# Performance work log

Hardware: AMD Instinct MI355X
Metric: run time of the kernel (lower is better)

## Reference

```python
import jax, jax.numpy as jnp
import numpy as np

BS, NQ, D = 4, 12500, 256
HEADS, LEVELS, POINTS = 8, 2, 4
HD = D // HEADS
D_FF = 2048
SHAPES = ((100, 100), (50, 50))   # (H, W) per level; sum(H*W) == NQ
STARTS = (0, 10000)


def layer_norm(x, g, b, eps=1e-5):
    m = x.mean(-1, keepdims=True)
    v = ((x - m) ** 2).mean(-1, keepdims=True)
    return (x - m) * jax.lax.rsqrt(v + eps) * g + b


def bilinear_sample(value_l, loc, H, W):
    # value_l: (bs, heads, H*W, hd); loc: (bs, heads, nq, P, 2) normalized [0,1]
    # matches F.grid_sample(align_corners=False, padding_mode='zeros')
    x = loc[..., 0] * W - 0.5
    y = loc[..., 1] * H - 0.5
    x0 = jnp.floor(x)
    y0 = jnp.floor(y)
    wx1 = x - x0
    wy1 = y - y0
    wx0 = 1.0 - wx1
    wy0 = 1.0 - wy1
    x0i = x0.astype(jnp.int32)
    y0i = y0.astype(jnp.int32)

    def gather(xi, yi):
        valid = (xi >= 0) & (xi < W) & (yi >= 0) & (yi < H)
        idx = jnp.clip(yi, 0, H - 1) * W + jnp.clip(xi, 0, W - 1)  # (bs,heads,nq,P)
        b, h, nq, P = idx.shape
        g = jnp.take_along_axis(value_l, idx.reshape(b, h, nq * P, 1), axis=2)
        g = g.reshape(b, h, nq, P, -1)
        return g * valid[..., None].astype(g.dtype)

    g00 = gather(x0i, y0i)
    g10 = gather(x0i + 1, y0i)
    g01 = gather(x0i, y0i + 1)
    g11 = gather(x0i + 1, y0i + 1)
    return (g00 * (wx0 * wy0)[..., None] + g10 * (wx1 * wy0)[..., None]
            + g01 * (wx0 * wy1)[..., None] + g11 * (wx1 * wy1)[..., None])


def setup_inputs() -> dict:
    key = jax.random.key(0)
    ks = jax.random.split(key, 20)
    s = 0.02
    inp = {
        'query': jax.random.normal(ks[0], (BS, NQ, D), jnp.float32),
        'reference_points': jax.random.uniform(ks[1], (BS, NQ, LEVELS, 2), jnp.float32),
        'w_off': s * jax.random.normal(ks[2], (D, HEADS * LEVELS * POINTS * 2), jnp.float32),
        'b_off': s * jax.random.normal(ks[3], (HEADS * LEVELS * POINTS * 2,), jnp.float32),
        'w_attn': s * jax.random.normal(ks[4], (D, HEADS * LEVELS * POINTS), jnp.float32),
        'b_attn': s * jax.random.normal(ks[5], (HEADS * LEVELS * POINTS,), jnp.float32),
        'w_val': s * jax.random.normal(ks[6], (D, D), jnp.float32),
        'b_val': jnp.zeros((D,), jnp.float32),
        'w_out': s * jax.random.normal(ks[7], (D, D), jnp.float32),
        'b_out': jnp.zeros((D,), jnp.float32),
        'w1': s * jax.random.normal(ks[8], (D, D_FF), jnp.float32),
        'b1': jnp.zeros((D_FF,), jnp.float32),
        'w2': s * jax.random.normal(ks[9], (D_FF, D), jnp.float32),
        'b2': jnp.zeros((D,), jnp.float32),
        'ln0_g': jnp.ones((D,), jnp.float32),
        'ln0_b': jnp.zeros((D,), jnp.float32),
        'ln1_g': jnp.ones((D,), jnp.float32),
        'ln1_b': jnp.zeros((D,), jnp.float32),
    }
    return inp


def reference(query, reference_points, w_off, b_off, w_attn, b_attn, w_val, b_val,
              w_out, b_out, w1, b1, w2, b2, ln0_g, ln0_b, ln1_g, ln1_b):
    bs, nq, _ = query.shape
    # value projection; encoder self-attention: value == query tokens
    value = (query @ w_val + b_val).reshape(bs, nq, HEADS, HD).transpose(0, 2, 1, 3)  # (bs,heads,nv,hd)
    off = (query @ w_off + b_off).reshape(bs, nq, HEADS, LEVELS, POINTS, 2)
    aw = (query @ w_attn + b_attn).reshape(bs, nq, HEADS, LEVELS * POINTS)
    aw = jax.nn.softmax(aw, axis=-1).reshape(bs, nq, HEADS, LEVELS, POINTS)

    out = jnp.zeros((bs, HEADS, nq, HD), query.dtype)
    for l, (H, W) in enumerate(SHAPES):
        normalizer = jnp.array([W, H], query.dtype)
        # (bs,nq,heads,P,2)
        loc = reference_points[:, :, None, l, None, :] + off[:, :, :, l] / normalizer
        loc = loc.transpose(0, 2, 1, 3, 4)  # (bs,heads,nq,P,2)
        v_l = value[:, :, STARTS[l]:STARTS[l] + H * W]  # (bs,heads,H*W,hd)
        sampled = bilinear_sample(v_l, loc, H, W)       # (bs,heads,nq,P,hd)
        w_l = aw[:, :, :, l].transpose(0, 2, 1, 3)      # (bs,heads,nq,P)
        out = out + (sampled * w_l[..., None]).sum(axis=3)

    attn_out = out.transpose(0, 2, 1, 3).reshape(bs, nq, D) @ w_out + b_out
    x = layer_norm(query + attn_out, ln0_g, ln0_b)
    h = jax.nn.relu(x @ w1 + b1)
    x = layer_norm(x + (h @ w2 + b2), ln1_g, ln1_b)
    return x
```

## Files before the change

### kernel.cpp

```cpp
#include <hip/hip_runtime.h>


#define NQv 12500
#define BSv 4
#define Dv  256
#define DFF 2048

typedef __attribute__((ext_vector_type(8))) __bf16 bf16x8;
typedef __attribute__((ext_vector_type(4))) float f32x4;

__device__ __forceinline__ ushort f32_to_bf16(float f) {
  unsigned u = __float_as_uint(f);
  u += 0x7FFFu + ((u >> 16) & 1u);
  return (ushort)(u >> 16);
}
__device__ __forceinline__ float bf16_to_f32(ushort u) {
  return __uint_as_float(((unsigned)u) << 16);
}

__global__ __launch_bounds__(256) void conv_bf16_kernel(
    const float* __restrict__ in, ushort* __restrict__ out, int n4) {
  int i = blockIdx.x * 256 + threadIdx.x;
  if (i >= n4) return;
  float4 v = reinterpret_cast<const float4*>(in)[i];
  uint2 st;
  st.x = (unsigned)f32_to_bf16(v.x) | ((unsigned)f32_to_bf16(v.y) << 16);
  st.y = (unsigned)f32_to_bf16(v.z) | ((unsigned)f32_to_bf16(v.w) << 16);
  reinterpret_cast<uint2*>(out)[i] = st;
}

__global__ __launch_bounds__(256) void ttrans_kernel(
    const float* __restrict__ in, ushort* __restrict__ out, int K, int N) {
  __shared__ ushort tl[64][65];
  const int n0 = blockIdx.x * 64, k0 = blockIdx.y * 64;
  const int t = threadIdx.x;
#pragma unroll
  for (int i = 0; i < 16; ++i) {
    int idx = t + 256 * i;
    int r = idx >> 6, c = idx & 63;
    tl[r][c] = f32_to_bf16(in[(size_t)(k0 + r) * N + n0 + c]);
  }
  __syncthreads();
#pragma unroll
  for (int i = 0; i < 16; ++i) {
    int idx = t + 256 * i;
    int r = idx >> 6, c = idx & 63;
    out[(size_t)(n0 + r) * K + k0 + c] = tl[c][r];
  }
}

__global__ __launch_bounds__(256) void build_wcat_kernel(
    const float* __restrict__ w_val, const float* __restrict__ w_off,
    const float* __restrict__ w_attn, const float* __restrict__ b_val,
    const float* __restrict__ b_off, const float* __restrict__ b_attn,
    ushort* __restrict__ wcat, float* __restrict__ bcat) {
  int i = blockIdx.x * 256 + threadIdx.x;
  if (i < 448 * 256) {
    int n = i >> 8, k = i & 255;
    float v = (n < 256) ? w_val[(size_t)k * 256 + n]
              : (n < 384) ? w_off[(size_t)k * 128 + (n - 256)]
                          : w_attn[(size_t)k * 64 + (n - 384)];
    wcat[i] = f32_to_bf16(v);
  }
  if (i < 512)
    bcat[i] = (i < 256) ? b_val[i] : (i < 384) ? b_off[i - 256]
              : (i < 448) ? b_attn[i - 384] : 0.f;
}

#define TBM 128
#define TBN 128
#define TBK 32

template <int RELU, int NMASK>
__global__ __launch_bounds__(256) void gemm128_kernel(
    const ushort* __restrict__ A, const ushort* __restrict__ Bt,
    const float* __restrict__ bias, ushort* __restrict__ C,
    int M, int K, int ldc, int Nreal) {
  __shared__ ushort lds[4][TBM * TBK];

  const int t = threadIdx.x;
  const int wid = t >> 6, lane = t & 63;
  const int wr = wid >> 1, wc = wid & 1;
  const int m0 = blockIdx.y * TBM;
  const int n0 = blockIdx.x * TBN;

  int srowA[2], srowB[2], gsl[2];
#pragma unroll
  for (int i = 0; i < 2; i++) {
    int row = i * 64 + (t >> 2);
    int ar = m0 + row;
    srowA[i] = (ar < M) ? ar : (M - 1);
    srowB[i] = n0 + row;
    gsl[i] = ((t & 3) ^ ((row >> 1) & 3)) * 8;
  }

  f32x4 acc[4][4] = {};
  const int nt = K / TBK;
  int cur = 0;

#pragma unroll
  for (int i = 0; i < 2; i++) {
    const int ldsoff = (i * 256 + wid * 64) * 8;
    __builtin_amdgcn_global_load_lds(
        (const __attribute__((address_space(1))) void*)(A + (size_t)srowA[i] * K + gsl[i]),
        (__attribute__((address_space(3))) void*)(lds[0] + ldsoff), 16, 0, 0);
    __builtin_amdgcn_global_load_lds(
        (const __attribute__((address_space(1))) void*)(Bt + (size_t)srowB[i] * K + gsl[i]),
        (__attribute__((address_space(3))) void*)(lds[1] + ldsoff), 16, 0, 0);
  }
  __syncthreads();

  const int rl = lane & 15, kh = lane >> 4;
  for (int tk = 0; tk < nt; ++tk) {
    if (tk + 1 < nt) {
      const int k0 = (tk + 1) * TBK;
      const int nb = (cur ^ 1) * 2;
#pragma unroll
      for (int i = 0; i < 2; i++) {
        const int ldsoff = (i * 256 + wid * 64) * 8;
        __builtin_amdgcn_global_load_lds(
            (const __attribute__((address_space(1))) void*)(A + (size_t)srowA[i] * K + k0 + gsl[i]),
            (__attribute__((address_space(3))) void*)(lds[nb] + ldsoff), 16, 0, 0);
        __builtin_amdgcn_global_load_lds(
            (const __attribute__((address_space(1))) void*)(Bt + (size_t)srowB[i] * K + k0 + gsl[i]),
            (__attribute__((address_space(3))) void*)(lds[nb + 1] + ldsoff), 16, 0, 0);
      }
    }
    {
      const ushort* As = lds[cur * 2];
      const ushort* Bs = lds[cur * 2 + 1];
      bf16x8 afr[4], bfr[4];
#pragma unroll
      for (int ni = 0; ni < 4; ni++) {
        int rowb = wc * 64 + ni * 16 + rl;
        int p = kh ^ ((rowb >> 1) & 3);
        bfr[ni] = *reinterpret_cast<const bf16x8*>(Bs + rowb * 32 + p * 8);
      }
#pragma unroll
      for (int mi = 0; mi < 4; mi++) {
        int rowa = wr * 64 + mi * 16 + rl;
        int p = kh ^ ((rowa >> 1) & 3);
        afr[mi] = *reinterpret_cast<const bf16x8*>(As + rowa * 32 + p * 8);
      }
#pragma unroll
      for (int mi = 0; mi < 4; mi++)
#pragma unroll
        for (int ni = 0; ni < 4; ni++)
          acc[mi][ni] = __builtin_amdgcn_mfma_f32_16x16x32_bf16(afr[mi], bfr[ni], acc[mi][ni], 0, 0, 0);
    }
    __syncthreads();
    cur ^= 1;
  }

  ushort* ldsC = lds[0];
  const int rgrp = lane >> 4, cl = lane & 15;
#pragma unroll
  for (int pass = 0; pass < 2; ++pass) {
    if (wr == pass) {
#pragma unroll
      for (int mi = 0; mi < 4; mi++) {
#pragma unroll
        for (int ni = 0; ni < 4; ni++) {
          int col = wc * 64 + ni * 16 + cl;
          float bv = bias[n0 + col];
#pragma unroll
          for (int r = 0; r < 4; r++) {
            int rloc = mi * 16 + rgrp * 4 + r;
            float v = acc[mi][ni][r] + bv;
            if (RELU) v = fmaxf(v, 0.f);
            ldsC[rloc * 132 + col] = f32_to_bf16(v);
          }
        }
      }
    }
    __syncthreads();
    {
      int rloc = t >> 2;
      int row = m0 + pass * 64 + rloc;
      if (row < M) {
#pragma unroll
        for (int j = 0; j < 4; j++) {
          int col = (t & 3) * 32 + j * 8;
          if (!NMASK || n0 + col < Nreal) {
            uint4 v = *reinterpret_cast<const uint4*>(ldsC + rloc * 132 + col);
            *reinterpret_cast<uint4*>(C + (size_t)row * ldc + n0 + col) = v;
          }
        }
      }
    }
    __syncthreads();
  }
}

__global__ __launch_bounds__(256, 2) void outproj_ln0_kernel(
    const ushort* __restrict__ samp,
    const ushort* __restrict__ wqt,
    const float* __restrict__ bias,
    const float* __restrict__ query,
    const float* __restrict__ g0, const float* __restrict__ be0,
    ushort* __restrict__ xb,
    int M) {
  __shared__ ushort lds_all[32768];
  ushort* As = lds_all;
  ushort* ring0 = lds_all + 16384;

  const int t = threadIdx.x;
  const int wv = t >> 6;
  const int lane = t & 63;
  const int rl = lane & 15, kq = lane >> 4;
  const int cl = lane & 15, g4 = lane >> 4;
  const int m0 = blockIdx.x * 64;

  ushort* ring[2] = {ring0, ring0 + 8192};

  auto issueB = [&](int j, ushort* dst) {
#pragma unroll
    for (int ii = 0; ii < 4; ++ii) {
      int row = (t >> 2) + 64 * ii;
      int g = (t & 3) ^ ((row >> 1) & 3);
      __builtin_amdgcn_global_load_lds(
          (const __attribute__((address_space(1))) void*)(
              wqt + (size_t)row * 256 + j * 32 + g * 8),
          (__attribute__((address_space(3))) void*)(dst + ((size_t)t + 256 * ii) * 8), 16, 0, 0);
    }
  };

#pragma unroll
  for (int ii = 0; ii < 8; ++ii) {
    int row = (t >> 5) + 8 * ii;
    int g = (t & 31) ^ (row & 7);
    int ar = m0 + row; ar = (ar < M) ? ar : (M - 1);
    __builtin_amdgcn_global_load_lds(
        (const __attribute__((address_space(1))) void*)(samp + (size_t)ar * 256 + g * 8),
        (__attribute__((address_space(3))) void*)(As + ((size_t)t + 256 * ii) * 8), 16, 0, 0);
  }
  issueB(0, ring[0]);
  __syncthreads();

  f32x4 accF[4][4] = {};
  int cur = 0;

#pragma unroll
  for (int j = 0; j < 8; ++j) {
    if (j + 1 < 8) issueB(j + 1, ring[cur ^ 1]);
    const ushort* Bs = ring[cur];
    bf16x8 afr[4], bfr[4];
    const int slotA = j * 4 + kq;
#pragma unroll
    for (int mi = 0; mi < 4; mi++) {
      int rowa = mi * 16 + rl;
      afr[mi] = *reinterpret_cast<const bf16x8*>(As + rowa * 256 + (slotA ^ (rowa & 7)) * 8);
    }
#pragma unroll
    for (int ni = 0; ni < 4; ni++) {
      int rowb = wv * 64 + ni * 16 + rl;
      bfr[ni] = *reinterpret_cast<const bf16x8*>(Bs + rowb * 32 + (kq ^ ((rowb >> 1) & 3)) * 8);
    }
    __builtin_amdgcn_s_setprio(1);
#pragma unroll
    for (int mi = 0; mi < 4; mi++)
#pragma unroll
      for (int ni = 0; ni < 4; ni++)
        accF[mi][ni] = __builtin_amdgcn_mfma_f32_16x16x32_bf16(afr[mi], bfr[ni], accF[mi][ni], 0, 0, 0);
    __builtin_amdgcn_s_setprio(0);
    __syncthreads();
    cur ^= 1;
  }

  float* ptab = (float*)ring0;
  float* mtab = (float*)(ring0 + 2048);

  float bc[4], gc[4], bec[4];
#pragma unroll
  for (int ni = 0; ni < 4; ni++) {
    int col = wv * 64 + ni * 16 + cl;
    bc[ni] = bias[col]; gc[ni] = g0[col]; bec[ni] = be0[col];
  }
#pragma unroll
  for (int mi = 0; mi < 4; mi++) {
#pragma unroll
    for (int ni = 0; ni < 4; ni++) {
      int col = wv * 64 + ni * 16 + cl;
#pragma unroll
      for (int r = 0; r < 4; r++) {
        int row = mi * 16 + g4 * 4 + r;
        int qrow = m0 + row; qrow = (qrow < M) ? qrow : (M - 1);
        accF[mi][ni][r] += bc[ni] + query[(size_t)qrow * 256 + col];
      }
    }
  }
#pragma unroll
  for (int mi = 0; mi < 4; mi++) {
#pragma unroll
    for (int r = 0; r < 4; r++) {
      float s = accF[mi][0][r] + accF[mi][1][r] + accF[mi][2][r] + accF[mi][3][r];
      float sq = accF[mi][0][r] * accF[mi][0][r] + accF[mi][1][r] * accF[mi][1][r] +
                 accF[mi][2][r] * accF[mi][2][r] + accF[mi][3][r] * accF[mi][3][r];
#pragma unroll
      for (int o = 1; o < 16; o <<= 1) {
        s += __shfl_xor(s, o, 64);
        sq += __shfl_xor(sq, o, 64);
      }
      if (cl == 0) {
        int row = mi * 16 + g4 * 4 + r;
        ptab[(row * 4 + wv) * 2 + 0] = s;
        ptab[(row * 4 + wv) * 2 + 1] = sq;
      }
    }
  }
  __syncthreads();
  {
    int row = t >> 2, part = t & 3;
    float s = ptab[(row * 4 + part) * 2 + 0];
    float sq = ptab[(row * 4 + part) * 2 + 1];
    s += __shfl_xor(s, 1, 64);  sq += __shfl_xor(sq, 1, 64);
    s += __shfl_xor(s, 2, 64);  sq += __shfl_xor(sq, 2, 64);
    if (part == 0) {
      float mean = s * (1.f / 256.f);
      float var = sq * (1.f / 256.f) - mean * mean;
      mtab[row * 2 + 0] = mean;
      mtab[row * 2 + 1] = rsqrtf(var + 1e-5f);
    }
  }
  __syncthreads();
#pragma unroll
  for (int mi = 0; mi < 4; mi++) {
#pragma unroll
    for (int r = 0; r < 4; r++) {
      int row = mi * 16 + g4 * 4 + r;
      float2 ms = *reinterpret_cast<const float2*>(mtab + row * 2);
      int grow = m0 + row;
      if (grow < M) {
#pragma unroll
        for (int ni = 0; ni < 4; ni++) {
          int col = wv * 64 + ni * 16 + cl;
          xb[(size_t)grow * 256 + col] =
              f32_to_bf16((accF[mi][ni][r] - ms.x) * ms.y * gc[ni] + bec[ni]);
        }
      }
    }
  }
}

__global__ __launch_bounds__(512, 1) void ffn_ln_fused_kernel(
    const ushort* __restrict__ xb,
    const ushort* __restrict__ w1t,
    const float* __restrict__ b1,
    const ushort* __restrict__ w2t,
    const float* __restrict__ b2,
    const float* __restrict__ g1, const float* __restrict__ be1,
    float* __restrict__ out,
    int M) {
  __shared__ ushort lds_all[74752];
  ushort* As = lds_all;
  ushort* Hs = lds_all + 32768;
  ushort* stg0 = lds_all + 50176;

  const int t = threadIdx.x;
  const int wv = t >> 6;
  const int wm = wv >> 2;
  const int wn = wv & 3;
  const int lane = t & 63;
  const int rl = lane & 15, kq = lane >> 4;
  const int cl = lane & 15, g4 = lane >> 4;
  const int m0 = blockIdx.x * 128;

  const int b1row = t >> 3, b1slot = t & 7;
  const int b2row = t >> 2, b2slot = t & 3;

  auto stg = [&](int i) { return stg0 + i * 8192; };

  auto issueB1 = [&](int p, int j, ushort* dst) {
#pragma unroll
    for (int ii = 0; ii < 2; ++ii) {
      int row = b1row + 64 * ii;
      int g = b1slot ^ (row & 7);
      __builtin_amdgcn_global_load_lds(
          (const __attribute__((address_space(1))) void*)(
              w1t + (size_t)(p * 128 + row) * 256 + j * 64 + g * 8),
          (__attribute__((address_space(3))) void*)(dst + (t + 512 * ii) * 8), 16, 0, 0);
    }
  };
  auto issueB2 = [&](int p, int tt, ushort* dst) {
#pragma unroll
    for (int ii = 0; ii < 2; ++ii) {
      int row = b2row + 128 * ii;
      int g = b2slot ^ ((row >> 1) & 3);
      __builtin_amdgcn_global_load_lds(
          (const __attribute__((address_space(1))) void*)(
              w2t + (size_t)row * 2048 + p * 128 + tt * 32 + g * 8),
          (__attribute__((address_space(3))) void*)(dst + (t + 512 * ii) * 8), 16, 0, 0);
    }
  };

#pragma unroll
  for (int ii = 0; ii < 8; ++ii) {
    int row = (t >> 5) + 16 * ii;
    int g = (t & 31) ^ (row & 7);
    int ar = m0 + row; ar = (ar < M) ? ar : (M - 1);
    __builtin_amdgcn_global_load_lds(
        (const __attribute__((address_space(1))) void*)(xb + (size_t)ar * 256 + g * 8),
        (__attribute__((address_space(3))) void*)(As + (t + 512 * ii) * 8), 16, 0, 0);
  }
  issueB1(0, 0, stg(0));
  issueB1(0, 1, stg(1));
  asm volatile("s_waitcnt vmcnt(2)" ::: "memory");
  __builtin_amdgcn_s_barrier();

  f32x4 acc1[4][2] = {};
  f32x4 accF[4][4] = {};
  int cur = 0;

  for (int p = 0; p < 16; ++p) {
#pragma unroll
    for (int j = 0; j < 8; ++j) {
      int tgt = cur + 2; if (tgt >= 3) tgt -= 3;
      if (j <= 5) {
        const int j2 = j + 2;
        const int p2 = p + (j2 >> 3);
        if ((j2 & 7) < 4) issueB1(p2, j2 & 3, stg(tgt));
        else issueB2(p2, (j2 & 7) - 4, stg(tgt));
        asm volatile("s_waitcnt vmcnt(4) lgkmcnt(0)" ::: "memory");
      } else if (p < 15) {
        const int j2m = (j + 2) & 7;
        issueB1(p + 1, j2m, stg(tgt));
        asm volatile("s_waitcnt vmcnt(4) lgkmcnt(0)" ::: "memory");
      } else if (j == 6) {
        asm volatile("s_waitcnt vmcnt(2) lgkmcnt(0)" ::: "memory");
      } else {
        asm volatile("s_waitcnt vmcnt(0) lgkmcnt(0)" ::: "memory");
      }
      __builtin_amdgcn_s_barrier();
      __builtin_amdgcn_sched_barrier(0);

      const ushort* Bs = stg(cur);
      if (j < 4) {
        __builtin_amdgcn_s_setprio(1);
#pragma unroll
        for (int kk = 0; kk < 2; ++kk) {
          bf16x8 afr[4], bfr[2];
          const int slotA = j * 8 + kk * 4 + kq;
#pragma unroll
          for (int mi = 0; mi < 4; mi++) {
            int rowa = wm * 64 + mi * 16 + rl;
            afr[mi] = *reinterpret_cast<const bf16x8*>(As + rowa * 256 + (slotA ^ (rowa & 7)) * 8);
          }
          const int slotB = kk * 4 + kq;
#pragma unroll
          for (int ni = 0; ni < 2; ni++) {
            int rowb = wn * 32 + ni * 16 + rl;
            bfr[ni] = *reinterpret_cast<const bf16x8*>(Bs + rowb * 64 + (slotB ^ (rowb & 7)) * 8);
          }
#pragma unroll
          for (int mi = 0; mi < 4; mi++)
#pragma unroll
            for (int ni = 0; ni < 2; ni++)
              acc1[mi][ni] = __builtin_amdgcn_mfma_f32_16x16x32_bf16(afr[mi], bfr[ni], acc1[mi][ni], 0, 0, 0);
        }
        __builtin_amdgcn_s_setprio(0);
        if (j == 3) {
#pragma unroll
          for (int ni = 0; ni < 2; ni++) {
            int col = wn * 32 + ni * 16 + cl;
            float b1v = b1[p * 128 + col];
#pragma unroll
            for (int mi = 0; mi < 4; mi++) {
#pragma unroll
              for (int r = 0; r < 4; r++) {
                int row = wm * 64 + mi * 16 + g4 * 4 + r;
                Hs[row * 136 + col] = f32_to_bf16(fmaxf(acc1[mi][ni][r] + b1v, 0.f));
              }
            }
          }
#pragma unroll
          for (int mi = 0; mi < 4; mi++)
#pragma unroll
            for (int ni = 0; ni < 2; ni++)
              acc1[mi][ni] = (f32x4){0.f, 0.f, 0.f, 0.f};
        }
      } else {
        const int tt = j - 4;
        bf16x8 a2f[4], b2f[4];
#pragma unroll
        for (int mi = 0; mi < 4; mi++) {
          int rowa = wm * 64 + mi * 16 + rl;
          a2f[mi] = *reinterpret_cast<const bf16x8*>(Hs + rowa * 136 + (tt * 4 + kq) * 8);
        }
#pragma unroll
        for (int ni = 0; ni < 4; ni++) {
          int rowb = wn * 64 + ni * 16 + rl;
          b2f[ni] = *reinterpret_cast<const bf16x8*>(Bs + rowb * 32 + (kq ^ ((rowb >> 1) & 3)) * 8);
        }
        __builtin_amdgcn_s_setprio(1);
#pragma unroll
        for (int mi = 0; mi < 4; mi++)
#pragma unroll
          for (int ni = 0; ni < 4; ni++)
            accF[mi][ni] = __builtin_amdgcn_mfma_f32_16x16x32_bf16(a2f[mi], b2f[ni], accF[mi][ni], 0, 0, 0);
        __builtin_amdgcn_s_setprio(0);
      }
      cur = cur + 1; if (cur >= 3) cur -= 3;
    }
  }

  float* ptab = (float*)stg0;
  float* mtab = (float*)(stg0 + 2048);

  float b2c[4], g1c[4], bec[4];
#pragma unroll
  for (int ni = 0; ni < 4; ni++) {
    int col = wn * 64 + ni * 16 + cl;
    b2c[ni] = b2[col]; g1c[ni] = g1[col]; bec[ni] = be1[col];
  }
#pragma unroll
  for (int mi = 0; mi < 4; mi++) {
#pragma unroll
    for (int ni = 0; ni < 4; ni++) {
      int col = wn * 64 + ni * 16 + cl;
#pragma unroll
      for (int r = 0; r < 4; r++) {
        int row = wm * 64 + mi * 16 + g4 * 4 + r;
        ushort xv = As[row * 256 + ((col >> 3) ^ (row & 7)) * 8 + (col & 7)];
        accF[mi][ni][r] += b2c[ni] + bf16_to_f32(xv);
      }
    }
  }
#pragma unroll
  for (int mi = 0; mi < 4; mi++) {
#pragma unroll
    for (int r = 0; r < 4; r++) {
      float s = accF[mi][0][r] + accF[mi][1][r] + accF[mi][2][r] + accF[mi][3][r];
      float sq = accF[mi][0][r] * accF[mi][0][r] + accF[mi][1][r] * accF[mi][1][r] +
                 accF[mi][2][r] * accF[mi][2][r] + accF[mi][3][r] * accF[mi][3][r];
#pragma unroll
      for (int o = 1; o < 16; o <<= 1) {
        s += __shfl_xor(s, o, 64);
        sq += __shfl_xor(sq, o, 64);
      }
      if (cl == 0) {
        int row = wm * 64 + mi * 16 + g4 * 4 + r;
        ptab[(row * 4 + wn) * 2 + 0] = s;
        ptab[(row * 4 + wn) * 2 + 1] = sq;
      }
    }
  }
  __syncthreads();
  {
    int row = t >> 2, part = t & 3;
    float s = ptab[(row * 4 + part) * 2 + 0];
    float sq = ptab[(row * 4 + part) * 2 + 1];
    s += __shfl_xor(s, 1, 64);  sq += __shfl_xor(sq, 1, 64);
    s += __shfl_xor(s, 2, 64);  sq += __shfl_xor(sq, 2, 64);
    if (part == 0) {
      float mean = s * (1.f / 256.f);
      float var = sq * (1.f / 256.f) - mean * mean;
      mtab[row * 2 + 0] = mean;
      mtab[row * 2 + 1] = rsqrtf(var + 1e-5f);
    }
  }
  __syncthreads();
#pragma unroll
  for (int mi = 0; mi < 4; mi++) {
#pragma unroll
    for (int r = 0; r < 4; r++) {
      int row = wm * 64 + mi * 16 + g4 * 4 + r;
      float2 ms = *reinterpret_cast<const float2*>(mtab + row * 2);
      int grow = m0 + row;
      if (grow < M) {
#pragma unroll
        for (int ni = 0; ni < 4; ni++) {
          int col = wn * 64 + ni * 16 + cl;
          out[(size_t)grow * 256 + col] = (accF[mi][ni][r] - ms.x) * ms.y * g1c[ni] + bec[ni];
        }
      }
    }
  }
}

__global__ __launch_bounds__(256) void deform_attn_kernel(
    const ushort* __restrict__ pcat, const float* __restrict__ refp,
    ushort* __restrict__ out, int total) {
  int tid = blockIdx.x * 256 + threadIdx.x;
  if (tid >= total) return;
  int c0 = (tid & 3) * 8;
  int idx = tid >> 2;
  int h = idx & 7;
  int row = idx >> 3;
  int bl = row / NQv;

  const ushort* prow = pcat + (size_t)row * 448;

  ushort awr[8];
  *reinterpret_cast<uint4*>(awr) = *reinterpret_cast<const uint4*>(prow + 384 + h * 8);
  float lg[8], mx = -1e30f;
#pragma unroll
  for (int i = 0; i < 8; i++) { lg[i] = bf16_to_f32(awr[i]); mx = fmaxf(mx, lg[i]); }
  float ssum = 0.f;
#pragma unroll
  for (int i = 0; i < 8; i++) { lg[i] = __expf(lg[i] - mx); ssum += lg[i]; }
  float inv = 1.f / ssum;

  ushort ofr[16];
  *reinterpret_cast<uint4*>(ofr)     = *reinterpret_cast<const uint4*>(prow + 256 + h * 16);
  *reinterpret_cast<uint4*>(ofr + 8) = *reinterpret_cast<const uint4*>(prow + 256 + h * 16 + 8);
  float4 rp = *reinterpret_cast<const float4*>(refp + (size_t)row * 4);

  float acc8[8] = {};
  const int Ws[2] = {100, 50}, Hs2[2] = {100, 50}, Ss[2] = {0, 10000};
#pragma unroll
  for (int l = 0; l < 2; l++) {
    const int W = Ws[l], H = Hs2[l];
    float fx = (l ? rp.z : rp.x) * (float)W - 0.5f;
    float fy = (l ? rp.w : rp.y) * (float)H - 0.5f;
    const ushort* vbase = pcat + ((size_t)bl * NQv + Ss[l]) * 448 + h * 32 + c0;
#pragma unroll
    for (int p = 0; p < 4; p++) {
      float x = fx + bf16_to_f32(ofr[l * 8 + p * 2 + 0]);
      float y = fy + bf16_to_f32(ofr[l * 8 + p * 2 + 1]);
      float x0f = floorf(x), y0f = floorf(y);
      float wx1 = x - x0f, wy1 = y - y0f;
      float wx0 = 1.f - wx1, wy0 = 1.f - wy1;
      int x0 = (int)x0f, y0 = (int)y0f;
      float aw = lg[l * 4 + p] * inv;

      float cw[4] = {aw * wx0 * wy0, aw * wx1 * wy0, aw * wx0 * wy1, aw * wx1 * wy1};
      int cx[4] = {x0, x0 + 1, x0, x0 + 1};
      int cy[4] = {y0, y0, y0 + 1, y0 + 1};
#pragma unroll
      for (int c = 0; c < 4; c++) {
        int xi = cx[c], yi = cy[c];
        if (xi >= 0 && xi < W && yi >= 0 && yi < H) {
          ushort vr[8];
          *reinterpret_cast<uint4*>(vr) =
              *reinterpret_cast<const uint4*>(vbase + (size_t)(yi * W + xi) * 448);
          float w = cw[c];
#pragma unroll
          for (int j = 0; j < 8; j++) acc8[j] += w * bf16_to_f32(vr[j]);
        }
      }
    }
  }

  ushort st[8];
#pragma unroll
  for (int j = 0; j < 8; j++) st[j] = f32_to_bf16(acc8[j]);
  *reinterpret_cast<uint4*>(out + (size_t)row * 256 + h * 32 + c0) =
      *reinterpret_cast<uint4*>(st);
}

extern "C" void kernel_launch(void* const* d_in, const int* in_sizes, int n_in,
                              void* d_out, int out_size, void* d_ws, size_t ws_size,
                              hipStream_t stream) {
  const float* query  = (const float*)d_in[0];
  const float* refp   = (const float*)d_in[1];
  const float* w_off  = (const float*)d_in[2];
  const float* b_off  = (const float*)d_in[3];
  const float* w_attn = (const float*)d_in[4];
  const float* b_attn = (const float*)d_in[5];
  const float* w_val  = (const float*)d_in[6];
  const float* b_val  = (const float*)d_in[7];
  const float* w_out  = (const float*)d_in[8];
  const float* b_out  = (const float*)d_in[9];
  const float* w1     = (const float*)d_in[10];
  const float* b1     = (const float*)d_in[11];
  const float* w2     = (const float*)d_in[12];
  const float* b2     = (const float*)d_in[13];
  const float* ln0g   = (const float*)d_in[14];
  const float* ln0b   = (const float*)d_in[15];
  const float* ln1g   = (const float*)d_in[16];
  const float* ln1b   = (const float*)d_in[17];
  float* outp = (float*)d_out;

  char* ws = (char*)d_ws;
  size_t woff = 0;
  auto walloc = [&](size_t bytes) { size_t r = woff; woff += (bytes + 255) & ~(size_t)255; return r; };
  ushort* wcat = (ushort*)(ws + walloc((size_t)512 * 256 * 2));
  float*  bcat = (float*)(ws + walloc(512 * 4));
  ushort* wqt  = (ushort*)(ws + walloc((size_t)256 * 256 * 2));
  ushort* w1t  = (ushort*)(ws + walloc((size_t)DFF * 256 * 2));
  ushort* w2t  = (ushort*)(ws + walloc((size_t)256 * DFF * 2));
  char* arena = ws + woff;
  size_t arena_sz = (ws_size > woff) ? (ws_size - woff) : 0;

  int nb = ((size_t)BSv * NQv * 1920 + (1u << 20) <= arena_sz) ? BSv : 1;
  const int R = nb * NQv;
  ushort* qb   = (ushort*)arena;
  ushort* pcat = (ushort*)(arena + (size_t)R * 512);
  ushort* samp = (ushort*)(arena + (size_t)R * 1408);
  ushort* xb   = qb;

  build_wcat_kernel<<<dim3(448), dim3(256), 0, stream>>>(
      w_val, w_off, w_attn, b_val, b_off, b_attn, wcat, bcat);
  ttrans_kernel<<<dim3(4, 4), dim3(256), 0, stream>>>(w_out, wqt, Dv, Dv);
  ttrans_kernel<<<dim3(DFF / 64, 4), dim3(256), 0, stream>>>(w1, w1t, Dv, DFF);
  ttrans_kernel<<<dim3(4, DFF / 64), dim3(256), 0, stream>>>(w2, w2t, DFF, Dv);

  const int MT = (R + TBM - 1) / TBM;

  for (int c = 0; c < BSv / nb; c++) {
    const int row0 = c * R;
    const float* qrow = query + (size_t)row0 * Dv;

    conv_bf16_kernel<<<dim3((R * 64 + 255) / 256), dim3(256), 0, stream>>>(qrow, qb, R * 64);

    gemm128_kernel<0, 1><<<dim3(4, MT), dim3(256), 0, stream>>>(
        qb, wcat, bcat, pcat, R, Dv, 448, 448);

    deform_attn_kernel<<<dim3((R * 32 + 255) / 256), dim3(256), 0, stream>>>(
        pcat, refp + (size_t)row0 * 4, samp, R * 32);

    outproj_ln0_kernel<<<dim3((R + 63) / 64), dim3(256), 0, stream>>>(
        samp, wqt, b_out, qrow, ln0g, ln0b, xb, R);

    ffn_ln_fused_kernel<<<dim3((R + 127) / 128), dim3(512), 0, stream>>>(
        xb, w1t, b1, w2t, b2, ln1g, ln1b, outp + (size_t)row0 * 256, R);
  }
}
```

Baseline: 328.9 us.

## Split value and offset/attn projections into separate buffers; share sampling work via shuffles

The fused projection GEMM now writes the value projection into a dense 256-wide buffer and the offsets plus attention logits into a separate 192-wide buffer, in place of one 448-wide interleaved array. Value gathers in the deformable attention kernel therefore stride 256 elements instead of 448, which packs sampled rows more tightly for cache and TLB. Each of the four lanes serving a head now loads only its share of offsets and logits, and the softmax and sample coordinates are exchanged with wave shuffles. This removes redundant per-lane loads and softmax work at the cost of extra shuffle instructions.

```diff
diff --git a/kernel.cpp b/kernel.cpp
--- a/kernel.cpp
+++ b/kernel.cpp
@@ -71,10 +71,11 @@
 #define TBN 128
 #define TBK 32
 
-template <int RELU, int NMASK>
+template <int RELU, int NMASK, int SPLIT>
 __global__ __launch_bounds__(256) void gemm128_kernel(
     const ushort* __restrict__ A, const ushort* __restrict__ Bt,
     const float* __restrict__ bias, ushort* __restrict__ C,
+    ushort* __restrict__ C2,
     int M, int K, int ldc, int Nreal) {
   __shared__ ushort lds[4][TBM * TBK];
 
@@ -181,8 +182,14 @@
 #pragma unroll
         for (int j = 0; j < 4; j++) {
           int col = (t & 3) * 32 + j * 8;
-          if (!NMASK || n0 + col < Nreal) {
-            uint4 v = *reinterpret_cast<const uint4*>(ldsC + rloc * 132 + col);
+          uint4 v = *reinterpret_cast<const uint4*>(ldsC + rloc * 132 + col);
+          if (SPLIT) {
+            int gcol = n0 + col;
+            if (gcol < 256)
+              *reinterpret_cast<uint4*>(C + (size_t)row * 256 + gcol) = v;
+            else if (gcol < 448)
+              *reinterpret_cast<uint4*>(C2 + (size_t)row * 192 + (gcol - 256)) = v;
+          } else if (!NMASK || n0 + col < Nreal) {
             *reinterpret_cast<uint4*>(C + (size_t)row * ldc + n0 + col) = v;
           }
         }
@@ -343,14 +350,10 @@
 }
 
 __global__ __launch_bounds__(512, 1) void ffn_ln_fused_kernel(
-    const ushort* __restrict__ xb,
-    const ushort* __restrict__ w1t,
-    const float* __restrict__ b1,
-    const ushort* __restrict__ w2t,
-    const float* __restrict__ b2,
-    const float* __restrict__ g1, const float* __restrict__ be1,
-    float* __restrict__ out,
-    int M) {
+    const ushort* __restrict__ xb, const ushort* __restrict__ w1t,
+    const float* __restrict__ b1, const ushort* __restrict__ w2t,
+    const float* __restrict__ b2, const float* __restrict__ g1,
+    const float* __restrict__ be1, float* __restrict__ out, int M) {
   __shared__ ushort lds_all[74752];
   ushort* As = lds_all;
   ushort* Hs = lds_all + 32768;
@@ -578,65 +581,73 @@
 }
 
 __global__ __launch_bounds__(256) void deform_attn_kernel(
-    const ushort* __restrict__ pcat, const float* __restrict__ refp,
-    ushort* __restrict__ out, int total) {
+    const ushort* __restrict__ val,
+    const ushort* __restrict__ oa,
+    const float* __restrict__ refp,
+    ushort* __restrict__ out,
+    int total)
+{
   int tid = blockIdx.x * 256 + threadIdx.x;
   if (tid >= total) return;
-  int c0 = (tid & 3) * 8;
+  int c = tid & 3;
   int idx = tid >> 2;
   int h = idx & 7;
   int row = idx >> 3;
   int bl = row / NQv;
 
-  const ushort* prow = pcat + (size_t)row * 448;
-
-  ushort awr[8];
-  *reinterpret_cast<uint4*>(awr) = *reinterpret_cast<const uint4*>(prow + 384 + h * 8);
-  float lg[8], mx = -1e30f;
-#pragma unroll
-  for (int i = 0; i < 8; i++) { lg[i] = bf16_to_f32(awr[i]); mx = fmaxf(mx, lg[i]); }
-  float ssum = 0.f;
-#pragma unroll
-  for (int i = 0; i < 8; i++) { lg[i] = __expf(lg[i] - mx); ssum += lg[i]; }
-  float inv = 1.f / ssum;
-
-  ushort ofr[16];
-  *reinterpret_cast<uint4*>(ofr)     = *reinterpret_cast<const uint4*>(prow + 256 + h * 16);
-  *reinterpret_cast<uint4*>(ofr + 8) = *reinterpret_cast<const uint4*>(prow + 256 + h * 16 + 8);
+  const ushort* orow = oa + (size_t)row * 192;
+
+  uint lraw = *reinterpret_cast<const uint*>(orow + 128 + h * 8 + c * 2);
+  float l0 = bf16_to_f32((ushort)(lraw & 0xffffu));
+  float l1 = bf16_to_f32((ushort)(lraw >> 16));
+  float mx = fmaxf(l0, l1);
+  mx = fmaxf(mx, __shfl_xor(mx, 1, 64));
+  mx = fmaxf(mx, __shfl_xor(mx, 2, 64));
+  float e0 = __expf(l0 - mx), e1 = __expf(l1 - mx);
+  float sm = e0 + e1;
+  sm += __shfl_xor(sm, 1, 64);
+  sm += __shfl_xor(sm, 2, 64);
+  float inv = 1.f / sm;
+
+  ushort o4[4];
+  *reinterpret_cast<uint2*>(o4) = *reinterpret_cast<const uint2*>(orow + h * 16 + c * 4);
   float4 rp = *reinterpret_cast<const float4*>(refp + (size_t)row * 4);
-
+  float Wl = (c & 2) ? 50.f : 100.f;
+  float fx = ((c & 2) ? rp.z : rp.x) * Wl - 0.5f;
+  float fy = ((c & 2) ? rp.w : rp.y) * Wl - 0.5f;
+  float myx0 = fx + bf16_to_f32(o4[0]);
+  float myy0 = fy + bf16_to_f32(o4[1]);
+  float myx1 = fx + bf16_to_f32(o4[2]);
+  float myy1 = fy + bf16_to_f32(o4[3]);
+  float myw0 = e0 * inv, myw1 = e1 * inv;
+
+  const int lanebase = (threadIdx.x & 63) & ~3;
   float acc8[8] = {};
-  const int Ws[2] = {100, 50}, Hs2[2] = {100, 50}, Ss[2] = {0, 10000};
-#pragma unroll
-  for (int l = 0; l < 2; l++) {
-    const int W = Ws[l], H = Hs2[l];
-    float fx = (l ? rp.z : rp.x) * (float)W - 0.5f;
-    float fy = (l ? rp.w : rp.y) * (float)H - 0.5f;
-    const ushort* vbase = pcat + ((size_t)bl * NQv + Ss[l]) * 448 + h * 32 + c0;
-#pragma unroll
-    for (int p = 0; p < 4; p++) {
-      float x = fx + bf16_to_f32(ofr[l * 8 + p * 2 + 0]);
-      float y = fy + bf16_to_f32(ofr[l * 8 + p * 2 + 1]);
-      float x0f = floorf(x), y0f = floorf(y);
-      float wx1 = x - x0f, wy1 = y - y0f;
-      float wx0 = 1.f - wx1, wy0 = 1.f - wy1;
-      int x0 = (int)x0f, y0 = (int)y0f;
-      float aw = lg[l * 4 + p] * inv;
-
-      float cw[4] = {aw * wx0 * wy0, aw * wx1 * wy0, aw * wx0 * wy1, aw * wx1 * wy1};
-      int cx[4] = {x0, x0 + 1, x0, x0 + 1};
-      int cy[4] = {y0, y0, y0 + 1, y0 + 1};
-#pragma unroll
-      for (int c = 0; c < 4; c++) {
-        int xi = cx[c], yi = cy[c];
-        if (xi >= 0 && xi < W && yi >= 0 && yi < H) {
-          ushort vr[8];
-          *reinterpret_cast<uint4*>(vr) =
-              *reinterpret_cast<const uint4*>(vbase + (size_t)(yi * W + xi) * 448);
-          float w = cw[c];
-#pragma unroll
-          for (int j = 0; j < 8; j++) acc8[j] += w * bf16_to_f32(vr[j]);
-        }
+#pragma unroll
+  for (int p = 0; p < 8; ++p) {
+    const int src = lanebase | (p >> 1);
+    float x = __shfl((p & 1) ? myx1 : myx0, src, 64);
+    float y = __shfl((p & 1) ? myy1 : myy0, src, 64);
+    float w = __shfl((p & 1) ? myw1 : myw0, src, 64);
+    const int W = (p < 4) ? 100 : 50, H = W;
+    const ushort* vbase = val + ((size_t)bl * NQv + ((p < 4) ? 0 : 10000)) * 256 + h * 32 + c * 8;
+    float x0f = floorf(x), y0f = floorf(y);
+    float wx1 = x - x0f, wy1 = y - y0f;
+    float wx0 = 1.f - wx1, wy0 = 1.f - wy1;
+    int x0 = (int)x0f, y0 = (int)y0f;
+    float cw[4] = {w * wx0 * wy0, w * wx1 * wy0, w * wx0 * wy1, w * wx1 * wy1};
+    int cx[4] = {x0, x0 + 1, x0, x0 + 1};
+    int cy[4] = {y0, y0, y0 + 1, y0 + 1};
+#pragma unroll
+    for (int cc = 0; cc < 4; cc++) {
+      int xi = cx[cc], yi = cy[cc];
+      if (xi >= 0 && xi < W && yi >= 0 && yi < H) {
+        ushort vr[8];
+        *reinterpret_cast<uint4*>(vr) =
+            *reinterpret_cast<const uint4*>(vbase + (size_t)(yi * W + xi) * 256);
+        float ww = cw[cc];
+#pragma unroll
+        for (int j = 0; j < 8; j++) acc8[j] += ww * bf16_to_f32(vr[j]);
       }
     }
   }
@@ -644,7 +655,7 @@
   ushort st[8];
 #pragma unroll
   for (int j = 0; j < 8; j++) st[j] = f32_to_bf16(acc8[j]);
-  *reinterpret_cast<uint4*>(out + (size_t)row * 256 + h * 32 + c0) =
+  *reinterpret_cast<uint4*>(out + (size_t)row * 256 + h * 32 + c * 8) =
       *reinterpret_cast<uint4*>(st);
 }
 
@@ -685,7 +696,8 @@
   int nb = ((size_t)BSv * NQv * 1920 + (1u << 20) <= arena_sz) ? BSv : 1;
   const int R = nb * NQv;
   ushort* qb   = (ushort*)arena;
-  ushort* pcat = (ushort*)(arena + (size_t)R * 512);
+  ushort* valb = (ushort*)(arena + (size_t)R * 512);
+  ushort* oab  = (ushort*)(arena + (size_t)R * 1024);
   ushort* samp = (ushort*)(arena + (size_t)R * 1408);
   ushort* xb   = qb;
 
@@ -703,11 +715,11 @@
 
     conv_bf16_kernel<<<dim3((R * 64 + 255) / 256), dim3(256), 0, stream>>>(qrow, qb, R * 64);
 
-    gemm128_kernel<0, 1><<<dim3(4, MT), dim3(256), 0, stream>>>(
-        qb, wcat, bcat, pcat, R, Dv, 448, 448);
+    gemm128_kernel<0, 1, 1><<<dim3(4, MT), dim3(256), 0, stream>>>(
+        qb, wcat, bcat, valb, oab, R, Dv, 448, 448);
 
     deform_attn_kernel<<<dim3((R * 32 + 255) / 256), dim3(256), 0, stream>>>(
-        pcat, refp + (size_t)row0 * 4, samp, R * 32);
+        valb, oab, refp + (size_t)row0 * 4, samp, R * 32);
 
     outproj_ln0_kernel<<<dim3((R + 63) / 64), dim3(256), 0, stream>>>(
         samp, wqt, b_out, qrow, ln0g, ln0b, xb, R);
```

After: 331.3 us. About the same (+0.7%).
